# Kernel tuning notes

Measured on AMD Instinct MI355X. Metric: run time of the kernel, lower is better.

The kernel has to match this reference:

```python
import jax, jax.numpy as jnp
import numpy as np

HEADS = 12
KEY_DIM = 16
B, C, H, W = 16, 384, 64, 64


def _hard_swish(x):
    return x * jnp.clip(x + 3.0, 0.0, 6.0) / 6.0


def _affine(x, g, b):
    # Inference-mode BatchNorm folded into per-channel scale/shift (NCHW).
    return x * g[:, None, None] + b[:, None, None]


def _pw(x, w):
    # 1x1 conv as a channel contraction: x [B,Cin,H,W], w [Cout,Cin].
    return jnp.einsum('bchw,oc->bohw', x, w)


def setup_inputs() -> dict:
    key = jax.random.key(0)
    ks = jax.random.split(key, 20)
    d = {}
    d['x'] = jax.random.normal(ks[0], (B, C, H, W), dtype=jnp.float32)
    d['rnd_offset'] = jax.random.uniform(ks[1], (B, 2, 1, 1), dtype=jnp.float32) * 6.0 - 3.0
    S = HEADS * KEY_DIM  # 192
    d['proj_w'] = jax.random.normal(ks[2], (3 * S, C + 2), dtype=jnp.float32) * 0.05
    d['proj_g'] = jax.random.uniform(ks[3], (3 * S,), dtype=jnp.float32) + 0.5
    d['proj_b'] = jax.random.normal(ks[4], (3 * S,), dtype=jnp.float32) * 0.1
    d['vp2_w'] = jax.random.normal(ks[5], (C, S), dtype=jnp.float32) * 0.05
    d['vp2_g'] = jax.random.uniform(ks[6], (C,), dtype=jnp.float32) + 0.5
    d['vp2_b'] = jax.random.normal(ks[7], (C,), dtype=jnp.float32) * 0.1
    d['dw_w'] = jax.random.normal(ks[8], (C, 1, 5, 5), dtype=jnp.float32) * 0.1
    d['dw_g'] = jax.random.uniform(ks[9], (C,), dtype=jnp.float32) + 0.5
    d['dw_b'] = jax.random.normal(ks[10], (C,), dtype=jnp.float32) * 0.1
    d['pw1_w'] = jax.random.normal(ks[11], (4 * C, C), dtype=jnp.float32) * 0.05
    d['pw1_g'] = jax.random.uniform(ks[12], (4 * C,), dtype=jnp.float32) + 0.5
    d['pw1_b'] = jax.random.normal(ks[13], (4 * C,), dtype=jnp.float32) * 0.1
    d['pw2_w'] = jax.random.normal(ks[14], (C, 4 * C), dtype=jnp.float32) * 0.05
    d['out_g'] = jax.random.uniform(ks[15], (C,), dtype=jnp.float32) + 0.5
    d['out_b'] = jax.random.normal(ks[16], (C,), dtype=jnp.float32) * 0.1
    d['rz_attn'] = jnp.float32(0.1)
    d['rz_ffn'] = jnp.float32(0.1)
    d['embed_strength'] = jnp.float32(-10.0)
    return d


def reference(x, rnd_offset, proj_w, proj_g, proj_b, vp2_w, vp2_g, vp2_b,
              dw_w, dw_g, dw_b, pw1_w, pw1_g, pw1_b, pw2_w, out_g, out_b,
              rz_attn, rz_ffn, embed_strength):
    b, c, h, w = x.shape
    # --- learned-strength positional embedding with random per-image offset ---
    xp = jnp.arange(w, dtype=x.dtype) / 1000.0
    yp = jnp.arange(h, dtype=x.dtype) / 1000.0
    xx, yy = jnp.meshgrid(xp, yp, indexing='xy')      # each (H, W)
    pos = jnp.stack([xx, yy], axis=0)[None]           # (1, 2, H, W)
    pos = jnp.exp(embed_strength) * (pos + rnd_offset)  # (B, 2, H, W)
    x_emb = jnp.concatenate([x, pos], axis=1)         # (B, C+2, H, W)

    # --- qkv projection (1x1 conv + BN + ReLU), computed in fp32 ---
    proj = jax.nn.relu(_affine(_pw(x_emb, proj_w), proj_g, proj_b))
    proj = proj.astype(jnp.float32)

    S = HEADS * KEY_DIM
    N = h * w

    def get_slice(i):
        # (B, S, H, W) slice -> (B*heads, N, key_dim)
        s = proj[:, i * S:(i + 1) * S]
        return s.reshape(b * HEADS, KEY_DIM, N).transpose(0, 2, 1)

    q, k, v = get_slice(0), get_slice(1), get_slice(2)

    # --- non-causal linear attention: Q (K^T V) / (Q sum(K)) ---
    ktv = jnp.einsum('bnd,bne->bde', k, v)            # (B*heads, d, d)
    numer = jnp.einsum('bnd,bde->bne', q, ktv)        # (B*heads, N, d)
    denom = jnp.einsum('bnd,bd->bn', q, k.sum(axis=1))[..., None]  # (B*heads, N, 1)
    out = numer / jnp.maximum(denom, 1e-4)
    out = out.transpose(0, 2, 1).reshape(b, S, h, w)  # (B, heads*key_dim, H, W)

    # --- value projection back to channels ---
    out = jax.nn.relu(_affine(_pw(out, vp2_w), vp2_g, vp2_b))
    y = x + rz_attn * out

    # --- FFN: depthwise 5x5 -> expand 1x1 -> project 1x1 (+ BNs) ---
    z = jax.lax.conv_general_dilated(
        y, dw_w, window_strides=(1, 1), padding='SAME',
        dimension_numbers=('NCHW', 'OIHW', 'NCHW'), feature_group_count=c)
    z = _hard_swish(_affine(z, dw_g, dw_b))
    z = _hard_swish(_affine(_pw(z, pw1_w), pw1_g, pw1_b))
    z = _affine(_pw(z, pw2_w), out_g, out_b)
    return y + rz_ffn * z
```

## Files before the change

### kernel.cpp

```cpp
#include <hip/hip_runtime.h>
#include <cstdint>

typedef unsigned short u16;
typedef __attribute__((ext_vector_type(8))) __bf16 bf16x8;
typedef __attribute__((ext_vector_type(4))) float f32x4;

__device__ __forceinline__ u16 f2bf(float f) {
    union { float f; uint32_t u; } v; v.f = f;
    uint32_t u = v.u;
    uint32_t r = (u + 0x7fffu + ((u >> 16) & 1u)) >> 16;
    return (u16)r;
}
__device__ __forceinline__ float bf2f(u16 h) {
    union { uint32_t u; float f; } v; v.u = ((uint32_t)h) << 16;
    return v.f;
}

__device__ __forceinline__ void ld_lds16(const u16* g, u16* l) {
    __builtin_amdgcn_global_load_lds(
        (const __attribute__((address_space(1))) uint32_t*)g,
        (__attribute__((address_space(3))) uint32_t*)l, 16, 0, 0);
}

__global__ __launch_bounds__(256) void prep(
    const float* __restrict__ proj_w, const float* __restrict__ proj_g,
    const float* __restrict__ proj_b, const float* __restrict__ vp2_w,
    const float* __restrict__ pw1_w, const float* __restrict__ pw2_w,
    const float* __restrict__ dw_w,
    u16* __restrict__ w1p, u16* __restrict__ w2, u16* __restrict__ w3,
    u16* __restrict__ w4, float* __restrict__ gp, float2* __restrict__ dwp)
{
    int i = blockIdx.x * 256 + threadIdx.x;
    if (i < 245760) {
        int o = i / 384, k = i - o * 384;
        w1p[i] = (o < 576) ? f2bf(proj_w[o * 386 + k]) : (u16)0;
        return;
    }
    i -= 245760;
    if (i < 73728) { w2[i] = f2bf(vp2_w[i]); return; }
    i -= 73728;
    if (i < 589824) { w3[i] = f2bf(pw1_w[i]); return; }
    i -= 589824;
    if (i < 589824) { w4[i] = f2bf(pw2_w[i]); return; }
    i -= 589824;
    if (i < 2560) {
        int which = i / 640, o = i - which * 640;
        float v = 0.f;
        if (o < 576) {
            v = (which == 0) ? proj_g[o] : (which == 1) ? proj_b[o]
                : (which == 2) ? proj_w[o * 386 + 384] : proj_w[o * 386 + 385];
        }
        gp[i] = v; return;
    }
    i -= 2560;
    if (i < 4800) {
        int tap = i / 192, cp = i - tap * 192;
        dwp[i] = make_float2(dw_w[(2 * cp) * 25 + tap], dw_w[(2 * cp + 1) * 25 + tap]);
    }
}

__global__ __launch_bounds__(256) void transpose_x(const float* __restrict__ x,
                                                   u16* __restrict__ xt)
{
    __shared__ float tile[64][65];
    int b = blockIdx.x, n0 = blockIdx.y * 64, c0 = blockIdx.z * 64;
    int t = threadIdx.x;
    int jj = t & 63, i0 = t >> 6;
    #pragma unroll
    for (int r = 0; r < 16; r++) {
        int ci = r * 4 + i0;
        tile[ci][jj] = x[((size_t)b * 384 + c0 + ci) * 4096 + n0 + jj];
    }
    __syncthreads();
    #pragma unroll
    for (int r = 0; r < 16; r++) {
        int ni = r * 4 + i0;
        xt[(size_t)(b * 4096 + n0 + ni) * 384 + c0 + jj] = f2bf(tile[jj][ni]);
    }
}

__global__ __launch_bounds__(256) void transpose_out(const u16* __restrict__ zf,
                                                     float* __restrict__ out)
{
    __shared__ float tile[64][65];
    int b = blockIdx.x, n0 = blockIdx.y * 64, c0 = blockIdx.z * 64;
    int t = threadIdx.x;
    int jj = t & 63, i0 = t >> 6;
    #pragma unroll
    for (int r = 0; r < 16; r++) {
        int ni = r * 4 + i0;
        tile[ni][jj] = bf2f(zf[(size_t)(b * 4096 + n0 + ni) * 384 + c0 + jj]);
    }
    __syncthreads();
    #pragma unroll
    for (int r = 0; r < 16; r++) {
        int ci = r * 4 + i0;
        out[((size_t)b * 384 + c0 + ci) * 4096 + n0 + jj] = tile[jj][ci];
    }
}

template <int MODE>
__global__ __launch_bounds__(256) void gemm_nhwc(
    const u16* __restrict__ A, const u16* __restrict__ W,
    u16* __restrict__ out, int K, int Osz, int nOT,
    const float* __restrict__ g, const float* __restrict__ bb,
    const float* __restrict__ w1x, const float* __restrict__ w1y,
    const u16* __restrict__ res, const float* __restrict__ sc,
    const float* __restrict__ rnd)
{
    constexpr int BK = 32;
    __shared__ u16 sA[3][128 * BK];
    __shared__ u16 sB[3][128 * BK];
    const int tid = threadIdx.x;
    const int lane = tid & 63;
    const int wv = tid >> 6;
    const int wm = (wv >> 1) * 64;
    const int wn = (wv & 1) * 64;

    const int nwg = gridDim.x;
    const int q8 = nwg >> 3;
    const int b1 = (blockIdx.x & 7) * q8 + (blockIdx.x >> 3);
    const int mt = b1 / nOT;
    const int ot = b1 - mt * nOT;
    const int m0 = mt * 128;
    const int o0 = ot * 128;

    const int q = lane >> 4;
    const int mr = lane & 15;
    const int ks = (q ^ ((mr >> 1) & 3)) * 8;

    const int tq = tid >> 2;
    const int sl = tid & 3;
    const int tk = (sl ^ ((tq >> 1) & 3)) * 8;
    const size_t ga0 = (size_t)(m0 + tq) * K + tk;
    const size_t ga1 = (size_t)(m0 + 64 + tq) * K + tk;
    const size_t gb0 = (size_t)(o0 + tq) * K + tk;
    const size_t gb1 = (size_t)(o0 + 64 + tq) * K + tk;
    const int lo0 = tq * BK + sl * 8;
    const int lo1 = (64 + tq) * BK + sl * 8;

    f32x4 acc[4][4] = {};
    const int nIter = K >> 5;

    ld_lds16(A + ga0, &sA[0][lo0]);
    ld_lds16(A + ga1, &sA[0][lo1]);
    ld_lds16(W + gb0, &sB[0][lo0]);
    ld_lds16(W + gb1, &sB[0][lo1]);
    if (nIter > 1) {
        ld_lds16(A + ga0 + BK, &sA[1][lo0]);
        ld_lds16(A + ga1 + BK, &sA[1][lo1]);
        ld_lds16(W + gb0 + BK, &sB[1][lo0]);
        ld_lds16(W + gb1 + BK, &sB[1][lo1]);
    }

    int buf = 0;
    for (int t = 0; t < nIter; ++t) {
        if (t + 1 < nIter) asm volatile("s_waitcnt vmcnt(4)" ::: "memory");
        else               asm volatile("s_waitcnt vmcnt(0)" ::: "memory");
        __builtin_amdgcn_s_barrier();
        __builtin_amdgcn_sched_barrier(0);
        if (t + 2 < nIter) {
            int nb = buf - 1; if (nb < 0) nb += 3;
            int k2 = (t + 2) * BK;
            ld_lds16(A + ga0 + k2, &sA[nb][lo0]);
            ld_lds16(A + ga1 + k2, &sA[nb][lo1]);
            ld_lds16(W + gb0 + k2, &sB[nb][lo0]);
            ld_lds16(W + gb1 + k2, &sB[nb][lo1]);
        }
        bf16x8 af[4], bfr[4];
        #pragma unroll
        for (int i = 0; i < 4; i++)
            af[i] = *(const bf16x8*)&sA[buf][(wm + i * 16 + mr) * BK + ks];
        #pragma unroll
        for (int j = 0; j < 4; j++)
            bfr[j] = *(const bf16x8*)&sB[buf][(wn + j * 16 + mr) * BK + ks];
        #pragma unroll
        for (int i = 0; i < 4; i++)
            #pragma unroll
            for (int j = 0; j < 4; j++)
                acc[i][j] = __builtin_amdgcn_mfma_f32_16x16x32_bf16(af[i], bfr[j], acc[i][j], 0, 0, 0);
        buf++; if (buf == 3) buf = 0;
    }

    float E = 0.f, offx = 0.f, offy = 0.f, rz = 0.f;
    if constexpr (MODE == 1) {
        E = expf(sc[0]);
        int bimg = m0 >> 12;
        offx = rnd[bimg * 2 + 0];
        offy = rnd[bimg * 2 + 1];
    }
    if constexpr (MODE == 2 || MODE == 4) rz = sc[0];

    #pragma unroll
    for (int j = 0; j < 4; j++) {
        int o = o0 + wn + j * 16 + mr;
        float gg = g[o], bbv = bb[o];
        float wx = 0.f, wy = 0.f;
        if constexpr (MODE == 1) { wx = w1x[o]; wy = w1y[o]; }
        #pragma unroll
        for (int i = 0; i < 4; i++) {
            #pragma unroll
            for (int r = 0; r < 4; r++) {
                int pix = m0 + wm + i * 16 + q * 4 + r;
                float v = acc[i][j][r];
                if constexpr (MODE == 1) {
                    int n = pix & 4095;
                    float px = E * ((float)(n & 63) * 0.001f + offx);
                    float py = E * ((float)(n >> 6) * 0.001f + offy);
                    v += px * wx + py * wy;
                    v = fmaxf(gg * v + bbv, 0.f);
                } else if constexpr (MODE == 2) {
                    v = fmaxf(gg * v + bbv, 0.f);
                    v = bf2f(res[(size_t)pix * 384 + o]) + rz * v;
                } else if constexpr (MODE == 3) {
                    float t = gg * v + bbv;
                    v = t * fminf(fmaxf(t + 3.f, 0.f), 6.f) * (1.f / 6.f);
                } else {
                    float t = gg * v + bbv;
                    v = bf2f(res[(size_t)pix * 384 + o]) + rz * t;
                }
                out[(size_t)pix * Osz + o] = f2bf(v);
            }
        }
    }
}

__global__ __launch_bounds__(256) void attn_ktv(const u16* __restrict__ proj,
                                                float* __restrict__ ktvp)
{
    int bh = blockIdx.x;
    int ch = blockIdx.y;
    int b = bh / 12, h = bh - b * 12;
    const u16* base = proj + (size_t)b * 4096 * 640;
    int kc = 192 + h * 16, vc = 384 + h * 16;
    __shared__ u16 ks[256 * 16];
    __shared__ u16 vs[256 * 16];
    int t = threadIdx.x;
    int d = t >> 4, e = t & 15;
    float acc = 0.f, ksum = 0.f;
    for (int n0 = ch * 1024; n0 < ch * 1024 + 1024; n0 += 256) {
        __syncthreads();
        const u16* r = base + (size_t)(n0 + t) * 640;
        ((float4*)&ks[t * 16])[0] = ((const float4*)(r + kc))[0];
        ((float4*)&ks[t * 16])[1] = ((const float4*)(r + kc))[1];
        ((float4*)&vs[t * 16])[0] = ((const float4*)(r + vc))[0];
        ((float4*)&vs[t * 16])[1] = ((const float4*)(r + vc))[1];
        __syncthreads();
        #pragma unroll 8
        for (int n = 0; n < 256; n++)
            acc += bf2f(ks[n * 16 + d]) * bf2f(vs[n * 16 + e]);
        if (t < 16) {
            #pragma unroll 8
            for (int n = 0; n < 256; n++) ksum += bf2f(ks[n * 16 + t]);
        }
    }
    float* o = ktvp + ((size_t)bh * 4 + ch) * 272;
    o[t] = acc;
    if (t < 16) o[256 + t] = ksum;
}

__global__ __launch_bounds__(256) void attn_apply(const u16* __restrict__ proj,
                                                  const float* __restrict__ ktvp,
                                                  u16* __restrict__ att)
{
    int bh = blockIdx.x;
    int b = bh / 12, h = bh - b * 12;
    __shared__ float kt[272];
    int t = threadIdx.x;
    {
        const float* p = ktvp + (size_t)bh * 4 * 272;
        kt[t] = p[t] + p[272 + t] + p[544 + t] + p[816 + t];
        if (t < 16) {
            int u = 256 + t;
            kt[u] = p[u] + p[272 + u] + p[544 + u] + p[816 + u];
        }
    }
    __syncthreads();
    int n = blockIdx.y * 256 + t;
    const u16* qr = proj + (size_t)(b * 4096 + n) * 640 + h * 16;
    float qv[16];
    #pragma unroll
    for (int d = 0; d < 16; d++) qv[d] = bf2f(qr[d]);
    float denom = 0.f;
    #pragma unroll
    for (int d = 0; d < 16; d++) denom += qv[d] * kt[256 + d];
    float rcp = 1.f / fmaxf(denom, 1e-4f);
    u16* op = att + (size_t)(b * 4096 + n) * 192 + h * 16;
    #pragma unroll
    for (int e = 0; e < 16; e++) {
        float s = 0.f;
        #pragma unroll
        for (int d = 0; d < 16; d++) s += qv[d] * kt[d * 16 + e];
        op[e] = f2bf(s * rcp);
    }
}

__global__ __launch_bounds__(192) void dwconv(const u16* __restrict__ y,
                                              const float2* __restrict__ wt,
                                              const float* __restrict__ g,
                                              const float* __restrict__ bc,
                                              u16* __restrict__ z)
{
    const int cp = threadIdx.x;
    const int xc = blockIdx.x;
    const int b  = blockIdx.y;
    const int c0 = cp * 2;

    float2 wv[25];
    #pragma unroll
    for (int t = 0; t < 25; t++) wv[t] = wt[t * 192 + cp];
    const float g0 = g[c0], g1 = g[c0 + 1];
    const float b0 = bc[c0], b1 = bc[c0 + 1];

    const size_t ibase = (size_t)b * 4096;
    const u16* ycol = y + ibase * 384 + c0;

    uint32_t r0[5], r1[5], r2[5], r3[5], r4[5];

#define LOADROW(yy, dst)                                                     \
    {                                                                        \
        if ((unsigned)(yy) < 64u) {                                          \
            const u16* rp = ycol + (size_t)(yy) * 64 * 384;                  \
            _Pragma("unroll")                                                \
            for (int dx = 0; dx < 5; dx++) {                                 \
                int xx = xc + dx - 2;                                        \
                dst[dx] = ((unsigned)xx < 64u)                               \
                              ? *(const uint32_t*)(rp + (size_t)xx * 384)    \
                              : 0u;                                          \
            }                                                                \
        } else {                                                             \
            _Pragma("unroll")                                                \
            for (int dx = 0; dx < 5; dx++) dst[dx] = 0u;                     \
        }                                                                    \
    }

#define COMPUTE(yr, A, B, C, D, E)                                           \
    if ((yr) < 64) {                                                         \
        float a0 = 0.f, a1 = 0.f;                                            \
        _Pragma("unroll")                                                    \
        for (int dx = 0; dx < 5; dx++) {                                     \
            uint32_t p;                                                      \
            p = A[dx];                                                       \
            a0 += wv[dx].x * bf2f((u16)(p & 0xffffu));                       \
            a1 += wv[dx].y * bf2f((u16)(p >> 16));                           \
            p = B[dx];                                                       \
            a0 += wv[5 + dx].x * bf2f((u16)(p & 0xffffu));                   \
            a1 += wv[5 + dx].y * bf2f((u16)(p >> 16));                       \
            p = C[dx];                                                       \
            a0 += wv[10 + dx].x * bf2f((u16)(p & 0xffffu));                  \
            a1 += wv[10 + dx].y * bf2f((u16)(p >> 16));                      \
            p = D[dx];                                                       \
            a0 += wv[15 + dx].x * bf2f((u16)(p & 0xffffu));                  \
            a1 += wv[15 + dx].y * bf2f((u16)(p >> 16));                      \
            p = E[dx];                                                       \
            a0 += wv[20 + dx].x * bf2f((u16)(p & 0xffffu));                  \
            a1 += wv[20 + dx].y * bf2f((u16)(p >> 16));                      \
        }                                                                    \
        float t0 = g0 * a0 + b0;                                             \
        float t1 = g1 * a1 + b1;                                             \
        t0 = t0 * fminf(fmaxf(t0 + 3.f, 0.f), 6.f) * (1.f / 6.f);            \
        t1 = t1 * fminf(fmaxf(t1 + 3.f, 0.f), 6.f) * (1.f / 6.f);            \
        uint32_t packed = (uint32_t)f2bf(t0) | ((uint32_t)f2bf(t1) << 16);   \
        *(uint32_t*)(z + (ibase + (size_t)(yr) * 64 + xc) * 384 + c0) = packed; \
    }

#define STEP(yr, A, B, C, D, E)                                              \
    COMPUTE(yr, A, B, C, D, E)                                               \
    LOADROW((yr) + 3, A)

    LOADROW(-2, r0)
    LOADROW(-1, r1)
    LOADROW(0, r2)
    LOADROW(1, r3)
    LOADROW(2, r4)

    for (int base = 0; base < 65; base += 5) {
        STEP(base + 0, r0, r1, r2, r3, r4)
        STEP(base + 1, r1, r2, r3, r4, r0)
        STEP(base + 2, r2, r3, r4, r0, r1)
        STEP(base + 3, r3, r4, r0, r1, r2)
        STEP(base + 4, r4, r0, r1, r2, r3)
    }
#undef STEP
#undef COMPUTE
#undef LOADROW
}

extern "C" void kernel_launch(void* const* d_in, const int* in_sizes, int n_in,
                              void* d_out, int out_size, void* d_ws, size_t ws_size,
                              hipStream_t stream)
{
    (void)in_sizes; (void)n_in; (void)out_size; (void)ws_size;
    const float* x       = (const float*)d_in[0];
    const float* rnd     = (const float*)d_in[1];
    const float* proj_w  = (const float*)d_in[2];
    const float* proj_g  = (const float*)d_in[3];
    const float* proj_b  = (const float*)d_in[4];
    const float* vp2_w   = (const float*)d_in[5];
    const float* vp2_g   = (const float*)d_in[6];
    const float* vp2_b   = (const float*)d_in[7];
    const float* dw_w    = (const float*)d_in[8];
    const float* dw_g    = (const float*)d_in[9];
    const float* dw_b    = (const float*)d_in[10];
    const float* pw1_w   = (const float*)d_in[11];
    const float* pw1_g   = (const float*)d_in[12];
    const float* pw1_b   = (const float*)d_in[13];
    const float* pw2_w   = (const float*)d_in[14];
    const float* out_g   = (const float*)d_in[15];
    const float* out_b   = (const float*)d_in[16];
    const float* rz_attn = (const float*)d_in[17];
    const float* rz_ffn  = (const float*)d_in[18];
    const float* es      = (const float*)d_in[19];
    float* out = (float*)d_out;

    char* ws = (char*)d_ws;
    u16*   xt   = (u16*)(ws + 0);
    u16*   att  = (u16*)(ws + 50331648);
    u16*   z2   = (u16*)(ws + 0);
    u16*   proj = (u16*)(ws + 201326592);
    u16*   z1   = proj;
    u16*   z4   = proj;
    u16*   yt   = (u16*)(ws + 285212672);
    u16*   w1p  = (u16*)(ws + 335753216);
    u16*   w2   = (u16*)(ws + 336244736);
    u16*   w3   = (u16*)(ws + 336392192);
    u16*   w4   = (u16*)(ws + 337571840);
    float* gp   = (float*)(ws + 338751488);
    float2* dwp = (float2*)(ws + 338761728);
    float* ktvp = (float*)(ws + 338800128);

    prep<<<5885, 256, 0, stream>>>(proj_w, proj_g, proj_b, vp2_w, pw1_w, pw2_w,
                                   dw_w, w1p, w2, w3, w4, gp, dwp);
    transpose_x<<<dim3(16, 64, 6), 256, 0, stream>>>(x, xt);
    gemm_nhwc<1><<<2560, 256, 0, stream>>>(xt, w1p, proj, 384, 640, 5,
        gp, gp + 640, gp + 1280, gp + 1920, nullptr, es, rnd);
    attn_ktv<<<dim3(192, 4), 256, 0, stream>>>(proj, ktvp);
    attn_apply<<<dim3(192, 16), 256, 0, stream>>>(proj, ktvp, att);
    gemm_nhwc<2><<<1536, 256, 0, stream>>>(att, w2, yt, 192, 384, 3,
        vp2_g, vp2_b, nullptr, nullptr, xt, rz_attn, nullptr);
    dwconv<<<dim3(64, 16), 192, 0, stream>>>(yt, dwp, dw_g, dw_b, z1);
    gemm_nhwc<3><<<6144, 256, 0, stream>>>(z1, w3, z2, 384, 1536, 12,
        pw1_g, pw1_b, nullptr, nullptr, nullptr, nullptr, nullptr);
    gemm_nhwc<4><<<1536, 256, 0, stream>>>(z2, w4, z4, 1536, 384, 3,
        out_g, out_b, nullptr, nullptr, yt, rz_ffn, nullptr);
    transpose_out<<<dim3(16, 64, 6), 256, 0, stream>>>(z4, out);
}
```

Baseline: 726.4 us.

## Load GEMM weight operand straight into registers, bypassing LDS

The weight (B) tile in the NHWC GEMM is no longer staged through a triple-buffered LDS array. Each wave now loads its MFMA B fragments from global memory into ping-pong registers, one K-step ahead, while the activation (A) tile keeps the LDS pipeline. The K loop is unrolled by two and wraps the MFMA block in s_setprio. This removes half the LDS traffic and shared-memory footprint, which may raise occupancy. In exchange, each lane reads strided 16-byte chunks across weight rows, and two waves redundantly fetch the same B rows. The unroll-by-two also assumes an even number of K iterations.

```diff
diff --git a/kernel.cpp b/kernel.cpp
--- a/kernel.cpp
+++ b/kernel.cpp
@@ -110,7 +110,6 @@
 {
     constexpr int BK = 32;
     __shared__ u16 sA[3][128 * BK];
-    __shared__ u16 sB[3][128 * BK];
     const int tid = threadIdx.x;
     const int lane = tid & 63;
     const int wv = tid >> 6;
@@ -134,53 +133,77 @@
     const int tk = (sl ^ ((tq >> 1) & 3)) * 8;
     const size_t ga0 = (size_t)(m0 + tq) * K + tk;
     const size_t ga1 = (size_t)(m0 + 64 + tq) * K + tk;
-    const size_t gb0 = (size_t)(o0 + tq) * K + tk;
-    const size_t gb1 = (size_t)(o0 + 64 + tq) * K + tk;
     const int lo0 = tq * BK + sl * 8;
     const int lo1 = (64 + tq) * BK + sl * 8;
 
+    const u16* wr0 = W + (size_t)(o0 + wn +  0 + mr) * K + q * 8;
+    const u16* wr1 = W + (size_t)(o0 + wn + 16 + mr) * K + q * 8;
+    const u16* wr2 = W + (size_t)(o0 + wn + 32 + mr) * K + q * 8;
+    const u16* wr3 = W + (size_t)(o0 + wn + 48 + mr) * K + q * 8;
+
     f32x4 acc[4][4] = {};
     const int nIter = K >> 5;
 
     ld_lds16(A + ga0, &sA[0][lo0]);
     ld_lds16(A + ga1, &sA[0][lo1]);
-    ld_lds16(W + gb0, &sB[0][lo0]);
-    ld_lds16(W + gb1, &sB[0][lo1]);
-    if (nIter > 1) {
-        ld_lds16(A + ga0 + BK, &sA[1][lo0]);
-        ld_lds16(A + ga1 + BK, &sA[1][lo1]);
-        ld_lds16(W + gb0 + BK, &sB[1][lo0]);
-        ld_lds16(W + gb1 + BK, &sB[1][lo1]);
-    }
+    ld_lds16(A + ga0 + BK, &sA[1][lo0]);
+    ld_lds16(A + ga1 + BK, &sA[1][lo1]);
+    bf16x8 bX0 = *(const bf16x8*)(wr0);
+    bf16x8 bX1 = *(const bf16x8*)(wr1);
+    bf16x8 bX2 = *(const bf16x8*)(wr2);
+    bf16x8 bX3 = *(const bf16x8*)(wr3);
+    bf16x8 bY0, bY1, bY2, bY3;
 
     int buf = 0;
-    for (int t = 0; t < nIter; ++t) {
-        if (t + 1 < nIter) asm volatile("s_waitcnt vmcnt(4)" ::: "memory");
-        else               asm volatile("s_waitcnt vmcnt(0)" ::: "memory");
-        __builtin_amdgcn_s_barrier();
-        __builtin_amdgcn_sched_barrier(0);
-        if (t + 2 < nIter) {
-            int nb = buf - 1; if (nb < 0) nb += 3;
-            int k2 = (t + 2) * BK;
-            ld_lds16(A + ga0 + k2, &sA[nb][lo0]);
-            ld_lds16(A + ga1 + k2, &sA[nb][lo1]);
-            ld_lds16(W + gb0 + k2, &sB[nb][lo0]);
-            ld_lds16(W + gb1 + k2, &sB[nb][lo1]);
-        }
-        bf16x8 af[4], bfr[4];
-        #pragma unroll
-        for (int i = 0; i < 4; i++)
-            af[i] = *(const bf16x8*)&sA[buf][(wm + i * 16 + mr) * BK + ks];
-        #pragma unroll
-        for (int j = 0; j < 4; j++)
-            bfr[j] = *(const bf16x8*)&sB[buf][(wn + j * 16 + mr) * BK + ks];
-        #pragma unroll
-        for (int i = 0; i < 4; i++)
-            #pragma unroll
-            for (int j = 0; j < 4; j++)
-                acc[i][j] = __builtin_amdgcn_mfma_f32_16x16x32_bf16(af[i], bfr[j], acc[i][j], 0, 0, 0);
-        buf++; if (buf == 3) buf = 0;
-    }
+
+#define GEMM_ITER(T, C0, C1, C2, C3, N0, N1, N2, N3)                         \
+    {                                                                        \
+        asm volatile("s_waitcnt vmcnt(6)" ::: "memory");                     \
+        __builtin_amdgcn_s_barrier();                                        \
+        __builtin_amdgcn_sched_barrier(0);                                   \
+        bf16x8 af0 = *(const bf16x8*)&sA[buf][(wm +  0 + mr) * BK + ks];     \
+        bf16x8 af1 = *(const bf16x8*)&sA[buf][(wm + 16 + mr) * BK + ks];     \
+        bf16x8 af2 = *(const bf16x8*)&sA[buf][(wm + 32 + mr) * BK + ks];     \
+        bf16x8 af3 = *(const bf16x8*)&sA[buf][(wm + 48 + mr) * BK + ks];     \
+        if ((T) + 2 < nIter) {         \
+            int nb = buf + 2; if (nb >= 3) nb -= 3;                          \
+            size_t ko = (size_t)((T) + 2) * BK;                              \
+            ld_lds16(A + ga0 + ko, &sA[nb][lo0]);                            \
+            ld_lds16(A + ga1 + ko, &sA[nb][lo1]);                            \
+        }                                                                    \
+        if ((T) + 1 < nIter) {            \
+            int kb = ((T) + 1) * BK;                                         \
+            N0 = *(const bf16x8*)(wr0 + kb);                                 \
+            N1 = *(const bf16x8*)(wr1 + kb);                                 \
+            N2 = *(const bf16x8*)(wr2 + kb);                                 \
+            N3 = *(const bf16x8*)(wr3 + kb);                                 \
+        }                                                                    \
+        __builtin_amdgcn_s_setprio(1);                                       \
+        acc[0][0] = __builtin_amdgcn_mfma_f32_16x16x32_bf16(af0, C0, acc[0][0], 0, 0, 0); \
+        acc[0][1] = __builtin_amdgcn_mfma_f32_16x16x32_bf16(af0, C1, acc[0][1], 0, 0, 0); \
+        acc[0][2] = __builtin_amdgcn_mfma_f32_16x16x32_bf16(af0, C2, acc[0][2], 0, 0, 0); \
+        acc[0][3] = __builtin_amdgcn_mfma_f32_16x16x32_bf16(af0, C3, acc[0][3], 0, 0, 0); \
+        acc[1][0] = __builtin_amdgcn_mfma_f32_16x16x32_bf16(af1, C0, acc[1][0], 0, 0, 0); \
+        acc[1][1] = __builtin_amdgcn_mfma_f32_16x16x32_bf16(af1, C1, acc[1][1], 0, 0, 0); \
+        acc[1][2] = __builtin_amdgcn_mfma_f32_16x16x32_bf16(af1, C2, acc[1][2], 0, 0, 0); \
+        acc[1][3] = __builtin_amdgcn_mfma_f32_16x16x32_bf16(af1, C3, acc[1][3], 0, 0, 0); \
+        acc[2][0] = __builtin_amdgcn_mfma_f32_16x16x32_bf16(af2, C0, acc[2][0], 0, 0, 0); \
+        acc[2][1] = __builtin_amdgcn_mfma_f32_16x16x32_bf16(af2, C1, acc[2][1], 0, 0, 0); \
+        acc[2][2] = __builtin_amdgcn_mfma_f32_16x16x32_bf16(af2, C2, acc[2][2], 0, 0, 0); \
+        acc[2][3] = __builtin_amdgcn_mfma_f32_16x16x32_bf16(af2, C3, acc[2][3], 0, 0, 0); \
+        acc[3][0] = __builtin_amdgcn_mfma_f32_16x16x32_bf16(af3, C0, acc[3][0], 0, 0, 0); \
+        acc[3][1] = __builtin_amdgcn_mfma_f32_16x16x32_bf16(af3, C1, acc[3][1], 0, 0, 0); \
+        acc[3][2] = __builtin_amdgcn_mfma_f32_16x16x32_bf16(af3, C2, acc[3][2], 0, 0, 0); \
+        acc[3][3] = __builtin_amdgcn_mfma_f32_16x16x32_bf16(af3, C3, acc[3][3], 0, 0, 0); \
+        __builtin_amdgcn_s_setprio(0);                                       \
+        buf++; if (buf == 3) buf = 0;                                        \
+    }
+
+    for (int t = 0; t < nIter; t += 2) {
+        GEMM_ITER(t,     bX0, bX1, bX2, bX3, bY0, bY1, bY2, bY3)
+        GEMM_ITER(t + 1, bY0, bY1, bY2, bY3, bX0, bX1, bX2, bX3)
+    }
+#undef GEMM_ITER
 
     float E = 0.f, offx = 0.f, offy = 0.f, rz = 0.f;
     if constexpr (MODE == 1) {
```

New measurement: 849.7 us. 1.17x slower.

## Stage GEMM epilogue through LDS for coalesced vectorized stores and raise MFMA priority

Applied to the files above, without the earlier changes.

The GEMM epilogue now writes accumulator tiles into LDS in four passes, then has each thread read a contiguous 16-channel row segment and emit 16-byte vectorized bf16 stores and residual loads. This replaces the scattered 2-byte per-element global stores and residual reads. Per-channel scale, shift and embedding weights are loaded once as float4 vectors. It also wraps the MFMA block in s_setprio and promotes the prefetch offset to size_t. The cost is extra barriers and LDS traffic in the epilogue.

```diff
diff --git a/kernel.cpp b/kernel.cpp
--- a/kernel.cpp
+++ b/kernel.cpp
@@ -160,8 +160,8 @@
         __builtin_amdgcn_s_barrier();
         __builtin_amdgcn_sched_barrier(0);
         if (t + 2 < nIter) {
-            int nb = buf - 1; if (nb < 0) nb += 3;
-            int k2 = (t + 2) * BK;
+            int nb = buf + 2; if (nb >= 3) nb -= 3;
+            size_t k2 = (size_t)(t + 2) * BK;
             ld_lds16(A + ga0 + k2, &sA[nb][lo0]);
             ld_lds16(A + ga1 + k2, &sA[nb][lo1]);
             ld_lds16(W + gb0 + k2, &sB[nb][lo0]);
@@ -174,13 +174,20 @@
         #pragma unroll
         for (int j = 0; j < 4; j++)
             bfr[j] = *(const bf16x8*)&sB[buf][(wn + j * 16 + mr) * BK + ks];
+        __builtin_amdgcn_s_setprio(1);
         #pragma unroll
         for (int i = 0; i < 4; i++)
             #pragma unroll
             for (int j = 0; j < 4; j++)
                 acc[i][j] = __builtin_amdgcn_mfma_f32_16x16x32_bf16(af[i], bfr[j], acc[i][j], 0, 0, 0);
+        __builtin_amdgcn_s_setprio(0);
         buf++; if (buf == 3) buf = 0;
     }
+
+    float* st = (float*)&sA[0][0];
+    const int wrh = wv >> 1;
+    const int row_l = tid >> 3;
+    const int cseg = (tid & 7) * 16;
 
     float E = 0.f, offx = 0.f, offy = 0.f, rz = 0.f;
     if constexpr (MODE == 1) {
@@ -191,37 +198,76 @@
     }
     if constexpr (MODE == 2 || MODE == 4) rz = sc[0];
 
-    #pragma unroll
-    for (int j = 0; j < 4; j++) {
-        int o = o0 + wn + j * 16 + mr;
-        float gg = g[o], bbv = bb[o];
-        float wx = 0.f, wy = 0.f;
-        if constexpr (MODE == 1) { wx = w1x[o]; wy = w1y[o]; }
-        #pragma unroll
-        for (int i = 0; i < 4; i++) {
+    const int ob = o0 + cseg;
+    float gv[16], bv[16];
+    #pragma unroll
+    for (int c = 0; c < 4; c++) {
+        *(float4*)&gv[c * 4] = *(const float4*)(g + ob + c * 4);
+        *(float4*)&bv[c * 4] = *(const float4*)(bb + ob + c * 4);
+    }
+    float wxv[16], wyv[16];
+    if constexpr (MODE == 1) {
+        #pragma unroll
+        for (int c = 0; c < 4; c++) {
+            *(float4*)&wxv[c * 4] = *(const float4*)(w1x + ob + c * 4);
+            *(float4*)&wyv[c * 4] = *(const float4*)(w1y + ob + c * 4);
+        }
+    }
+
+    #pragma unroll
+    for (int p = 0; p < 4; ++p) {
+        __syncthreads();
+        if (wrh == (p >> 1)) {
+            const int ib = (p & 1) * 2;
             #pragma unroll
-            for (int r = 0; r < 4; r++) {
-                int pix = m0 + wm + i * 16 + q * 4 + r;
-                float v = acc[i][j][r];
-                if constexpr (MODE == 1) {
-                    int n = pix & 4095;
-                    float px = E * ((float)(n & 63) * 0.001f + offx);
-                    float py = E * ((float)(n >> 6) * 0.001f + offy);
-                    v += px * wx + py * wy;
-                    v = fmaxf(gg * v + bbv, 0.f);
-                } else if constexpr (MODE == 2) {
-                    v = fmaxf(gg * v + bbv, 0.f);
-                    v = bf2f(res[(size_t)pix * 384 + o]) + rz * v;
-                } else if constexpr (MODE == 3) {
-                    float t = gg * v + bbv;
-                    v = t * fminf(fmaxf(t + 3.f, 0.f), 6.f) * (1.f / 6.f);
-                } else {
-                    float t = gg * v + bbv;
-                    v = bf2f(res[(size_t)pix * 384 + o]) + rz * t;
-                }
-                out[(size_t)pix * Osz + o] = f2bf(v);
+            for (int ii = 0; ii < 2; ++ii)
+                #pragma unroll
+                for (int j = 0; j < 4; ++j)
+                    #pragma unroll
+                    for (int r = 0; r < 4; ++r)
+                        st[(ii * 16 + q * 4 + r) * 130 + wn + j * 16 + mr] =
+                            acc[ib + ii][j][r];
+        }
+        __syncthreads();
+        const int pix = m0 + p * 32 + row_l;
+        float vals[16];
+        #pragma unroll
+        for (int e = 0; e < 16; ++e) vals[e] = st[row_l * 130 + cseg + e];
+
+        u16 rv[16];
+        if constexpr (MODE == 2 || MODE == 4) {
+            #pragma unroll
+            for (int c = 0; c < 2; c++)
+                *(float4*)&rv[c * 8] = *(const float4*)(res + (size_t)pix * 384 + ob + c * 8);
+        }
+        float px = 0.f, py = 0.f;
+        if constexpr (MODE == 1) {
+            int n = pix & 4095;
+            px = E * ((float)(n & 63) * 0.001f + offx);
+            py = E * ((float)(n >> 6) * 0.001f + offy);
+        }
+        u16 ov[16];
+        #pragma unroll
+        for (int e = 0; e < 16; ++e) {
+            float v = vals[e];
+            if constexpr (MODE == 1) {
+                v += px * wxv[e] + py * wyv[e];
+                v = fmaxf(gv[e] * v + bv[e], 0.f);
+            } else if constexpr (MODE == 2) {
+                v = fmaxf(gv[e] * v + bv[e], 0.f);
+                v = bf2f(rv[e]) + rz * v;
+            } else if constexpr (MODE == 3) {
+                float tv = gv[e] * v + bv[e];
+                v = tv * fminf(fmaxf(tv + 3.f, 0.f), 6.f) * (1.f / 6.f);
+            } else {
+                float tv = gv[e] * v + bv[e];
+                v = bf2f(rv[e]) + rz * tv;
             }
-        }
+            ov[e] = f2bf(v);
+        }
+        #pragma unroll
+        for (int c = 0; c < 2; c++)
+            *(float4*)(out + (size_t)pix * Osz + ob + c * 8) = *(const float4*)&ov[c * 8];
     }
 }
 
```

Measured after the change: 704.2 us. 3.1% less time.
